# Performance work log

Hardware: AMD Instinct MI355X
Metric: run time of the kernel (lower is better)

## Reference

```python
import jax, jax.numpy as jnp
import numpy as np

NUM_NODES = 100000
NUM_EDGES = 500000
HID = 256


def setup_inputs() -> dict:
    key = jax.random.key(0)
    ks = jax.random.split(key, 6)
    emb_src = jax.random.normal(ks[0], (NUM_NODES, HID), dtype=jnp.float32)
    emb_dst = jax.random.normal(ks[1], (NUM_NODES, HID), dtype=jnp.float32)
    edge_label_index = jax.random.randint(ks[2], (2, NUM_EDGES), 0, NUM_NODES, dtype=jnp.int32)
    # torch Linear(2H, H) weight is [H, 2H]; we store transposed [2H, H] for x @ W
    W1 = jax.random.normal(ks[3], (2 * HID, HID), dtype=jnp.float32) * (1.0 / np.sqrt(2 * HID))
    b1 = jnp.zeros((HID,), dtype=jnp.float32)
    W2 = jax.random.normal(ks[4], (HID, 1), dtype=jnp.float32) * (1.0 / np.sqrt(HID))
    b2 = jnp.zeros((1,), dtype=jnp.float32)
    return {"emb_src": emb_src, "emb_dst": emb_dst, "edge_label_index": edge_label_index,
            "W1": W1, "b1": b1, "W2": W2, "b2": b2}


def reference(emb_src, emb_dst, edge_label_index, W1, b1, W2, b2):
    # decode(): gather src/dst embeddings, concat, Linear-ReLU-Linear, squeeze
    src_idx = edge_label_index[0]
    dst_idx = edge_label_index[1]
    h_src = emb_src[src_idx]          # [E, H] irregular gather
    h_dst = emb_dst[dst_idx]          # [E, H]
    # concat([h_src, h_dst]) @ W1 == h_src @ W1[:H] + h_dst @ W1[H:]
    # (avoids materializing the [E, 2H] concatenated tensor)
    h = jnp.dot(h_src, W1[:HID]) + jnp.dot(h_dst, W1[HID:]) + b1  # [E, H]
    h = jax.nn.relu(h)
    logits = (jnp.dot(h, W2) + b2)[:, 0]  # [E]
    return logits
```

## Files before the change

### kernel.cpp

```cpp
#include <hip/hip_runtime.h>
#include <hip/hip_bf16.h>
#include <stdint.h>

#define HID 256
#define BM  64
#define LDA 68
#define LDC 264

typedef __bf16 bf16x8 __attribute__((ext_vector_type(8)));
typedef float  f32x4  __attribute__((ext_vector_type(4)));

__device__ __forceinline__ ushort f2bf(float x) {
    union { float f; uint32_t u; } v; v.f = x;
    uint32_t u = v.u;
    uint32_t r = u + 0x7fffu + ((u >> 16) & 1u);
    return (ushort)(r >> 16);
}

__device__ __forceinline__ uint32_t pack2bf(float a, float b) {
    union { float f; uint32_t u; } ua, ub;
    ua.f = a; ub.f = b;
    return __builtin_amdgcn_perm(ub.u + 0x8000u, ua.u + 0x8000u, 0x07060302u);
}

__device__ __forceinline__ float uaf(uint32_t x) {
    union { uint32_t u; float f; } c; c.u = x; return c.f;
}

__global__ void conv_w1(const float* __restrict__ W1, ushort* __restrict__ Wt4) {
    __shared__ ushort tr[32][33];
    const int bk = blockIdx.x >> 3;
    const int bn = blockIdx.x & 7;
    const int t  = threadIdx.x;
    #pragma unroll
    for (int i = 0; i < 4; ++i) {
        int e = t + 256 * i; int r = e >> 5, cc = e & 31;
        tr[cc][r] = f2bf(W1[(size_t)(bk * 32 + r) * HID + bn * 32 + cc]);
    }
    __syncthreads();
    #pragma unroll
    for (int i = 0; i < 4; ++i) {
        int e = t + 256 * i; int rn = e >> 5, ck = e & 31;
        int k = bk * 32 + ck;
        int grp = k >> 3;
        int j   = k & 7;
        int n   = bn * 32 + rn;
        Wt4[((size_t)grp * HID + n) * 8 + j] = tr[rn][ck];
    }
}

__global__ __launch_bounds__(256, 3)
void node_gemm(const float* __restrict__ emb0, const float* __restrict__ emb1,
               const ushort* __restrict__ Wt4,
               ushort* __restrict__ u0, ushort* __restrict__ u1,
               int n0, int n1, int nb0) {
    __shared__ ushort Cs[BM * LDC];

    const int t    = threadIdx.x;
    const int tb   = (blockIdx.x >= nb0) ? 1 : 0;
    const int bloc = blockIdx.x - tb * nb0;
    const float*  emb = tb ? emb1 : emb0;
    ushort*       uo  = tb ? u1 : u0;
    const int     n   = tb ? n1 : n0;
    const int     e0  = bloc * BM;

    const int wave = t >> 6, lane = t & 63, q = lane >> 4, cl = lane & 15;

    const float* arow[4];
    #pragma unroll
    for (int mi = 0; mi < 4; ++mi) {
        int r = e0 + mi * 16 + cl; if (r > n - 1) r = n - 1;
        arow[mi] = emb + (size_t)r * HID + q * 8;
    }
    const ushort* bb = Wt4 + ((size_t)q * HID + wave * 64 + cl) * 8;

    f32x4 acc[4][4] = {};

    #pragma unroll
    for (int c = 0; c < 4; ++c) {
        bf16x8 bfr[2][4];
        #pragma unroll
        for (int ks = 0; ks < 2; ++ks)
            #pragma unroll
            for (int ni = 0; ni < 4; ++ni)
                bfr[ks][ni] = *reinterpret_cast<const bf16x8*>(
                    bb + (((size_t)((tb * 4 + c) * 2 + ks) * 4) * HID + ni * 16) * 8);
        float4 a0[2][4], a1[2][4];
        #pragma unroll
        for (int ks = 0; ks < 2; ++ks)
            #pragma unroll
            for (int mi = 0; mi < 4; ++mi) {
                const float* p = arow[mi] + c * 64 + ks * 32;
                a0[ks][mi] = *reinterpret_cast<const float4*>(p);
                a1[ks][mi] = *reinterpret_cast<const float4*>(p + 4);
            }
        #pragma unroll
        for (int ks = 0; ks < 2; ++ks)
            #pragma unroll
            for (int mi = 0; mi < 4; ++mi) {
                union { uint32_t d[4]; bf16x8 v; } af;
                af.d[0] = pack2bf(a0[ks][mi].x, a0[ks][mi].y);
                af.d[1] = pack2bf(a0[ks][mi].z, a0[ks][mi].w);
                af.d[2] = pack2bf(a1[ks][mi].x, a1[ks][mi].y);
                af.d[3] = pack2bf(a1[ks][mi].z, a1[ks][mi].w);
                #pragma unroll
                for (int ni = 0; ni < 4; ++ni)
                    acc[mi][ni] = __builtin_amdgcn_mfma_f32_16x16x32_bf16(
                        af.v, bfr[ks][ni], acc[mi][ni], 0, 0, 0);
            }
    }

    #pragma unroll
    for (int mi = 0; mi < 4; ++mi)
        #pragma unroll
        for (int ni = 0; ni < 4; ++ni)
            #pragma unroll
            for (int r = 0; r < 4; ++r)
                Cs[(mi * 16 + q * 4 + r) * LDC + wave * 64 + ni * 16 + cl] =
                    f2bf(acc[mi][ni][r]);
    __syncthreads();

    const int srow = t >> 2, scol = (t & 3) * 64;
    if (e0 + srow < n) {
        ushort* dst = uo + (size_t)(e0 + srow) * HID + scol;
        #pragma unroll
        for (int i = 0; i < 8; ++i) {
            uint4 w = *reinterpret_cast<const uint4*>(&Cs[srow * LDC + scol + i * 8]);
            *reinterpret_cast<uint4*>(dst + i * 8) = w;
        }
    }
}

__global__ __launch_bounds__(256, 8)
void lp_edge(const ushort* __restrict__ u, const ushort* __restrict__ v,
             const int* __restrict__ eli,
             const float* __restrict__ b1, const float* __restrict__ W2,
             const float* __restrict__ b2, float* __restrict__ out,
             int E, int nwaves) {
    const int lane = threadIdx.x & 63;
    const int half = lane >> 5, sub = lane & 31;
    const int wid  = blockIdx.x * (blockDim.x >> 6) + (threadIdx.x >> 6);

    float b1v[8], w2v[8];
    {
        const float4* p1 = reinterpret_cast<const float4*>(b1 + sub * 8);
        const float4* p2 = reinterpret_cast<const float4*>(W2 + sub * 8);
        float4 a = p1[0], b = p1[1], c = p2[0], d = p2[1];
        b1v[0]=a.x; b1v[1]=a.y; b1v[2]=a.z; b1v[3]=a.w;
        b1v[4]=b.x; b1v[5]=b.y; b1v[6]=b.z; b1v[7]=b.w;
        w2v[0]=c.x; w2v[1]=c.y; w2v[2]=c.z; w2v[3]=c.w;
        w2v[4]=d.x; w2v[5]=d.y; w2v[6]=d.z; w2v[7]=d.w;
    }
    const float bias2 = b2[0];
    const ushort* tab  = half ? v : u;
    const int*    idxp = eli + (size_t)half * E;

    for (int base = wid * 8; base < E; base += nwaves * 8) {
        uint4 g[8];
        #pragma unroll
        for (int j = 0; j < 8; ++j) {
            int e = base + j; if (e > E - 1) e = E - 1;
            int row = idxp[e];
            g[j] = *reinterpret_cast<const uint4*>(tab + (size_t)row * HID + sub * 8);
        }
        float res = 0.f;
        #pragma unroll
        for (int j = 0; j < 8; ++j) {
            uint32_t pd[4], gd[4] = { g[j].x, g[j].y, g[j].z, g[j].w };
            #pragma unroll
            for (int c = 0; c < 4; ++c) pd[c] = (uint32_t)__shfl_xor((int)gd[c], 32);
            float acc = 0.f;
            #pragma unroll
            for (int c = 0; c < 4; ++c) {
                float a0 = uaf(gd[c] << 16), a1 = uaf(gd[c] & 0xffff0000u);
                float o0 = uaf(pd[c] << 16), o1 = uaf(pd[c] & 0xffff0000u);
                float h0 = fmaxf(a0 + o0 + b1v[2 * c], 0.f);
                float h1 = fmaxf(a1 + o1 + b1v[2 * c + 1], 0.f);
                acc = fmaf(h0, w2v[2 * c], acc);
                acc = fmaf(h1, w2v[2 * c + 1], acc);
            }
            #pragma unroll
            for (int m = 1; m <= 16; m <<= 1) acc += __shfl_xor(acc, m);
            if (half == 0 && sub == j) res = acc + bias2;
        }
        int e = base + sub;
        if (half == 0 && sub < 8 && e < E) out[e] = res;
    }
}

__global__ __launch_bounds__(256, 3)
void lp_mono(const float* __restrict__ es, const float* __restrict__ ed,
             const int* __restrict__ eli, const float* __restrict__ W1,
             const float* __restrict__ b1, const float* __restrict__ W2,
             const float* __restrict__ b2,
             float* __restrict__ out, int E) {
    __shared__ __align__(16) ushort As[2][BM * LDA];
    __shared__ int   sIdx[2][BM];
    __shared__ float hred[4][BM];

    const int t = threadIdx.x, e0 = blockIdx.x * BM;
    const int wave = t >> 6, lane = t & 63, q = lane >> 4, cl = lane & 15;

    if (t < 2 * BM) {
        int which = t >> 6, e = t & 63;
        int ge = e0 + e; if (ge > E - 1) ge = E - 1;
        sIdx[which][e] = eli[which * E + ge];
    }
    __syncthreads();

    int ge_[2], go_[2], rsrc[2], rdst[2];
    #pragma unroll
    for (int i = 0; i < 2; ++i) {
        int c2 = t + 256 * i;
        ge_[i] = c2 >> 3; go_[i] = c2 & 7;
        rsrc[i] = sIdx[0][ge_[i]];
        rdst[i] = sIdx[1][ge_[i]];
    }
    float4 g0[2], g1[2];
    auto gather = [&](int c) {
        const float* tab = (c < 4) ? es : ed;
        #pragma unroll
        for (int i = 0; i < 2; ++i) {
            int row = (c < 4) ? rsrc[i] : rdst[i];
            const float* p = tab + (size_t)row * HID + (c & 3) * 64 + go_[i] * 8;
            g0[i] = *reinterpret_cast<const float4*>(p);
            g1[i] = *reinterpret_cast<const float4*>(p + 4);
        }
    };
    auto cvstore = [&](int buf) {
        #pragma unroll
        for (int i = 0; i < 2; ++i) {
            uint4 v;
            v.x = pack2bf(g0[i].x, g0[i].y); v.y = pack2bf(g0[i].z, g0[i].w);
            v.z = pack2bf(g1[i].x, g1[i].y); v.w = pack2bf(g1[i].z, g1[i].w);
            *reinterpret_cast<uint4*>(&As[buf][ge_[i] * LDA + go_[i] * 8]) = v;
        }
    };
    gather(0); cvstore(0); __syncthreads();
    f32x4 acc[4][4] = {};
    #pragma unroll
    for (int c = 0; c < 8; ++c) {
        const int cur = c & 1;
        if (c < 7) gather(c + 1);
        #pragma unroll
        for (int ks = 0; ks < 2; ++ks) {
            bf16x8 af[4], bfr[4];
            #pragma unroll
            for (int mi = 0; mi < 4; ++mi)
                af[mi] = *reinterpret_cast<const bf16x8*>(
                    &As[cur][(mi * 16 + cl) * LDA + ks * 32 + q * 8]);
            #pragma unroll
            for (int ni = 0; ni < 4; ++ni) {
                int nn = wave * 64 + ni * 16 + cl;
                union { ushort s[8]; bf16x8 v; } u;
                #pragma unroll
                for (int j = 0; j < 8; ++j)
                    u.s[j] = f2bf(W1[(size_t)(c * 64 + ks * 32 + q * 8 + j) * HID + nn]);
                bfr[ni] = u.v;
            }
            #pragma unroll
            for (int mi = 0; mi < 4; ++mi)
                #pragma unroll
                for (int ni = 0; ni < 4; ++ni)
                    acc[mi][ni] = __builtin_amdgcn_mfma_f32_16x16x32_bf16(
                        af[mi], bfr[ni], acc[mi][ni], 0, 0, 0);
        }
        if (c < 7) { cvstore(cur ^ 1); __syncthreads(); }
    }
    float b1v[4], w2v[4];
    #pragma unroll
    for (int ni = 0; ni < 4; ++ni) {
        int col = wave * 64 + ni * 16 + cl;
        b1v[ni] = b1[col]; w2v[ni] = W2[col];
    }
    #pragma unroll
    for (int mi = 0; mi < 4; ++mi) {
        #pragma unroll
        for (int r = 0; r < 4; ++r) {
            float s = 0.f;
            #pragma unroll
            for (int ni = 0; ni < 4; ++ni) {
                float h = acc[mi][ni][r] + b1v[ni];
                h = fmaxf(h, 0.f);
                s += h * w2v[ni];
            }
            s += __shfl_xor(s, 1); s += __shfl_xor(s, 2);
            s += __shfl_xor(s, 4); s += __shfl_xor(s, 8);
            if (cl == 0) hred[wave][mi * 16 + q * 4 + r] = s;
        }
    }
    __syncthreads();
    if (t < BM) {
        int ge = e0 + t;
        if (ge < E)
            out[ge] = hred[0][t] + hred[1][t] + hred[2][t] + hred[3][t] + b2[0];
    }
}

extern "C" void kernel_launch(void* const* d_in, const int* in_sizes, int n_in,
                              void* d_out, int out_size, void* d_ws, size_t ws_size,
                              hipStream_t stream) {
    const float* emb_src = (const float*)d_in[0];
    const float* emb_dst = (const float*)d_in[1];
    const int*   eli     = (const int*)d_in[2];
    const float* W1      = (const float*)d_in[3];
    const float* b1      = (const float*)d_in[4];
    const float* W2      = (const float*)d_in[5];
    const float* b2      = (const float*)d_in[6];
    float*       out     = (float*)d_out;

    const int E   = in_sizes[2] / 2;
    const int n0n = in_sizes[0] / HID;
    const int n1n = in_sizes[1] / HID;

    const size_t wtB = (size_t)2 * HID * 2 * HID * sizeof(ushort);
    const size_t uB  = (size_t)n0n * HID * sizeof(ushort);
    const size_t vB  = (size_t)n1n * HID * sizeof(ushort);

    ushort* Wt4 = (ushort*)d_ws;
    ushort* u0  = (ushort*)((char*)d_ws + wtB);
    ushort* u1  = (ushort*)((char*)d_ws + wtB + uB);

    const int fullPath = ws_size >= wtB + uB + vB;

    if (fullPath) {
        conv_w1<<<128, 256, 0, stream>>>(W1, Wt4);
        const int nb0 = (n0n + BM - 1) / BM;
        const int nb1 = (n1n + BM - 1) / BM;
        node_gemm<<<nb0 + nb1, 256, 0, stream>>>(emb_src, emb_dst, Wt4,
                                                 u0, u1, n0n, n1n, nb0);
        const int eb = 2048;
        lp_edge<<<eb, 256, 0, stream>>>(u0, u1, eli, b1, W2, b2, out, E, eb * 4);
    } else {
        const int nb = (E + BM - 1) / BM;
        lp_mono<<<nb, 256, 0, stream>>>(emb_src, emb_dst, eli, W1,
                                        b1, W2, b2, out, E);
    }
}
```

Before: 392.9 us.

## Stage node GEMM A tiles through double-buffered LDS with coalesced loads

The node GEMM no longer loads fp32 embedding rows straight into MFMA fragment registers with strided per-lane reads. It now gathers coalesced float4 rows, converts them to bf16, and stores them into a double-buffered LDS tile, prefetching the next K chunk while MFMAs run on the current one. The output write-back is reorganised so consecutive threads write consecutive 16-byte units of a row. Separately, the edge kernel's occupancy hint drops from 8 to 4 and its grid is halved. The costs are extra LDS traffic and barriers in the GEMM, plus a possible loss of latency hiding in the edge kernel.

```diff
diff --git a/kernel.cpp b/kernel.cpp
--- a/kernel.cpp
+++ b/kernel.cpp
@@ -54,7 +54,10 @@
                const ushort* __restrict__ Wt4,
                ushort* __restrict__ u0, ushort* __restrict__ u1,
                int n0, int n1, int nb0) {
-    __shared__ ushort Cs[BM * LDC];
+    __shared__ __align__(16) union {
+        ushort As[2][BM * LDA];
+        ushort Cs[BM * LDC];
+    } sm;
 
     const int t    = threadIdx.x;
     const int tb   = (blockIdx.x >= nb0) ? 1 : 0;
@@ -66,72 +69,90 @@
 
     const int wave = t >> 6, lane = t & 63, q = lane >> 4, cl = lane & 15;
 
-    const float* arow[4];
-    #pragma unroll
-    for (int mi = 0; mi < 4; ++mi) {
-        int r = e0 + mi * 16 + cl; if (r > n - 1) r = n - 1;
-        arow[mi] = emb + (size_t)r * HID + q * 8;
-    }
-    const ushort* bb = Wt4 + ((size_t)q * HID + wave * 64 + cl) * 8;
+    const int r0  = t >> 4, seg = t & 15;
+    int rcl[4];
+    #pragma unroll
+    for (int i = 0; i < 4; ++i) {
+        int r = e0 + r0 + 16 * i; if (r > n - 1) r = n - 1;
+        rcl[i] = r;
+    }
+    const float* abase = emb + seg * 4;
+    const int    sbase = r0 * LDA + seg * 4;
+
+    float4 g[4];
+    auto gather = [&](int c) {
+        #pragma unroll
+        for (int i = 0; i < 4; ++i)
+            g[i] = *reinterpret_cast<const float4*>(abase + (size_t)rcl[i] * HID + c * 64);
+    };
+    auto cvstore = [&](int buf) {
+        #pragma unroll
+        for (int i = 0; i < 4; ++i) {
+            uint2 v;
+            v.x = pack2bf(g[i].x, g[i].y);
+            v.y = pack2bf(g[i].z, g[i].w);
+            *reinterpret_cast<uint2*>(&sm.As[buf][sbase + i * 16 * LDA]) = v;
+        }
+    };
+
+    gather(0); cvstore(0);
+    __syncthreads();
 
     f32x4 acc[4][4] = {};
 
     #pragma unroll
     for (int c = 0; c < 4; ++c) {
+        const int cur = c & 1;
         bf16x8 bfr[2][4];
         #pragma unroll
-        for (int ks = 0; ks < 2; ++ks)
+        for (int ks = 0; ks < 2; ++ks) {
+            const ushort* bb = Wt4 + ((size_t)(tb * 32 + c * 8 + ks * 4 + q) * HID) * 8;
             #pragma unroll
             for (int ni = 0; ni < 4; ++ni)
                 bfr[ks][ni] = *reinterpret_cast<const bf16x8*>(
-                    bb + (((size_t)((tb * 4 + c) * 2 + ks) * 4) * HID + ni * 16) * 8);
-        float4 a0[2][4], a1[2][4];
-        #pragma unroll
-        for (int ks = 0; ks < 2; ++ks)
-            #pragma unroll
-            for (int mi = 0; mi < 4; ++mi) {
-                const float* p = arow[mi] + c * 64 + ks * 32;
-                a0[ks][mi] = *reinterpret_cast<const float4*>(p);
-                a1[ks][mi] = *reinterpret_cast<const float4*>(p + 4);
-            }
-        #pragma unroll
-        for (int ks = 0; ks < 2; ++ks)
-            #pragma unroll
-            for (int mi = 0; mi < 4; ++mi) {
-                union { uint32_t d[4]; bf16x8 v; } af;
-                af.d[0] = pack2bf(a0[ks][mi].x, a0[ks][mi].y);
-                af.d[1] = pack2bf(a0[ks][mi].z, a0[ks][mi].w);
-                af.d[2] = pack2bf(a1[ks][mi].x, a1[ks][mi].y);
-                af.d[3] = pack2bf(a1[ks][mi].z, a1[ks][mi].w);
+                    bb + (wave * 64 + ni * 16 + cl) * 8);
+        }
+        if (c < 3) gather(c + 1);
+        #pragma unroll
+        for (int ks = 0; ks < 2; ++ks) {
+            bf16x8 af[4];
+            #pragma unroll
+            for (int mi = 0; mi < 4; ++mi)
+                af[mi] = *reinterpret_cast<const bf16x8*>(
+                    &sm.As[cur][(mi * 16 + cl) * LDA + ks * 32 + q * 8]);
+            #pragma unroll
+            for (int mi = 0; mi < 4; ++mi)
                 #pragma unroll
                 for (int ni = 0; ni < 4; ++ni)
                     acc[mi][ni] = __builtin_amdgcn_mfma_f32_16x16x32_bf16(
-                        af.v, bfr[ks][ni], acc[mi][ni], 0, 0, 0);
-            }
-    }
-
+                        af[mi], bfr[ks][ni], acc[mi][ni], 0, 0, 0);
+        }
+        if (c < 3) { cvstore(cur ^ 1); __syncthreads(); }
+    }
+
+    __syncthreads();
     #pragma unroll
     for (int mi = 0; mi < 4; ++mi)
         #pragma unroll
         for (int ni = 0; ni < 4; ++ni)
             #pragma unroll
             for (int r = 0; r < 4; ++r)
-                Cs[(mi * 16 + q * 4 + r) * LDC + wave * 64 + ni * 16 + cl] =
+                sm.Cs[(mi * 16 + q * 4 + r) * LDC + wave * 64 + ni * 16 + cl] =
                     f2bf(acc[mi][ni][r]);
     __syncthreads();
 
-    const int srow = t >> 2, scol = (t & 3) * 64;
-    if (e0 + srow < n) {
-        ushort* dst = uo + (size_t)(e0 + srow) * HID + scol;
-        #pragma unroll
-        for (int i = 0; i < 8; ++i) {
-            uint4 w = *reinterpret_cast<const uint4*>(&Cs[srow * LDC + scol + i * 8]);
-            *reinterpret_cast<uint4*>(dst + i * 8) = w;
-        }
-    }
-}
-
-__global__ __launch_bounds__(256, 8)
+    #pragma unroll
+    for (int i = 0; i < 8; ++i) {
+        int f = t + 256 * i;
+        int row = f >> 5, unit = f & 31;
+        if (e0 + row < n) {
+            uint4 w = *reinterpret_cast<const uint4*>(&sm.Cs[row * LDC + unit * 8]);
+            *reinterpret_cast<uint4*>(uo + (size_t)(e0 + row) * HID + unit * 8) = w;
+        }
+    }
+}
+
+__global__ __launch_bounds__(256, 4)
 void lp_edge(const ushort* __restrict__ u, const ushort* __restrict__ v,
              const int* __restrict__ eli,
              const float* __restrict__ b1, const float* __restrict__ W2,
@@ -329,7 +350,7 @@
         const int nb1 = (n1n + BM - 1) / BM;
         node_gemm<<<nb0 + nb1, 256, 0, stream>>>(emb_src, emb_dst, Wt4,
                                                  u0, u1, n0n, n1n, nb0);
-        const int eb = 2048;
+        const int eb = 1024;
         lp_edge<<<eb, 256, 0, stream>>>(u0, u1, eli, b1, W2, b2, out, E, eb * 4);
     } else {
         const int nb = (E + BM - 1) / BM;
```

New measurement: 322.5 us. 1.22x faster.
